# Kernel tuning notes

Measured on AMD Instinct MI355X. Metric: run time of the kernel, lower is better.

## Reference

```python
import jax, jax.numpy as jnp
import numpy as np

N, K, D = 100000, 8, 128
EPS = 1e-08


def setup_inputs() -> dict:
    key = jax.random.key(0)
    ks = jax.random.split(key, K)
    return {f"h{i}": jax.random.normal(ks[i], (N, D), dtype=jnp.float32) for i in range(K)}


def reference(h0, h1, h2, h3, h4, h5, h6, h7):
    # stack heads: [N, K, D] (matches torch.stack(head_outputs, dim=1))
    x = jnp.stack([h0, h1, h2, h3, h4, h5, h6, h7], axis=1)
    # F.normalize(p=2, dim=1, eps): x / max(||x||_2, eps) per (node, head) row
    norm = jnp.linalg.norm(x, axis=-1, keepdims=True)
    xn = x / jnp.maximum(norm, EPS)
    # per-node cross-correlation: [N, K, K]
    cc = jnp.einsum('nkd,nld->nkl', xn, xn)
    diff = cc - jnp.eye(K, dtype=cc.dtype)  # broadcasts over N
    # mean over nodes of sum of squared off-identity entries
    return jnp.sum(diff * diff) / N
```

## Files before the change

### kernel.cpp

```cpp
#include <hip/hip_runtime.h>


#define EPS 1e-8f

constexpr int D = 128;
constexpr int BLOCK = 64;
constexpr int NODES_PER_BLOCK = 16;

__global__ __launch_bounds__(BLOCK) void btd_main(
    const float* __restrict__ h0, const float* __restrict__ h1,
    const float* __restrict__ h2, const float* __restrict__ h3,
    const float* __restrict__ h4, const float* __restrict__ h5,
    const float* __restrict__ h6, const float* __restrict__ h7,
    float* __restrict__ partials, int n_nodes)
{
    const int lane = threadIdx.x & 63;
    const int g    = lane >> 2;
    const int l    = lane & 3;
    const int node = blockIdx.x * NODES_PER_BLOCK + g;

    float acc[36];
    #pragma unroll
    for (int i = 0; i < 36; ++i) acc[i] = 0.f;

    const unsigned base = (unsigned)node * D + l * 4;
    #pragma unroll
    for (int i = 0; i < 8; ++i) {
        const unsigned off = base + i * 16;
        float4 v[8];
        v[0] = *reinterpret_cast<const float4*>(h0 + off);
        v[1] = *reinterpret_cast<const float4*>(h1 + off);
        v[2] = *reinterpret_cast<const float4*>(h2 + off);
        v[3] = *reinterpret_cast<const float4*>(h3 + off);
        v[4] = *reinterpret_cast<const float4*>(h4 + off);
        v[5] = *reinterpret_cast<const float4*>(h5 + off);
        v[6] = *reinterpret_cast<const float4*>(h6 + off);
        v[7] = *reinterpret_cast<const float4*>(h7 + off);
        int idx = 0;
        #pragma unroll
        for (int k = 0; k < 8; ++k) {
            #pragma unroll
            for (int m = k; m < 8; ++m) {
                acc[idx] += v[k].x * v[m].x + v[k].y * v[m].y
                          + v[k].z * v[m].z + v[k].w * v[m].w;
                ++idx;
            }
        }
    }

    #pragma unroll
    for (int i = 0; i < 36; ++i) {
        acc[i] += __shfl_xor(acc[i], 1, 64);
        acc[i] += __shfl_xor(acc[i], 2, 64);
    }

    float inv[8];
    float loss = 0.f;
    #pragma unroll
    for (int k = 0; k < 8; ++k) {
        const int dk = k * (17 - k) / 2;
        inv[k] = rsqrtf(fmaxf(acc[dk], EPS * EPS));
        const float dterm = acc[dk] * inv[k] * inv[k] - 1.0f;
        loss += dterm * dterm;
    }
    #pragma unroll
    for (int k = 0; k < 8; ++k) {
        #pragma unroll
        for (int m = k + 1; m < 8; ++m) {
            const float cc = acc[k * (17 - k) / 2 + (m - k)] * inv[k] * inv[m];
            loss += 2.0f * cc * cc;
        }
    }
    loss *= 0.25f;

    #pragma unroll
    for (int off = 32; off > 0; off >>= 1)
        loss += __shfl_down(loss, off, 64);
    if (lane == 0) partials[blockIdx.x] = loss;
}

__global__ __launch_bounds__(256) void btd_reduce(
    const float* __restrict__ partials, int nparts,
    float* __restrict__ out, float inv_n)
{
    float s = 0.f;
    for (int i = threadIdx.x; i < nparts; i += 256) s += partials[i];
    #pragma unroll
    for (int off = 32; off > 0; off >>= 1) s += __shfl_down(s, off, 64);
    __shared__ float smem[4];
    const int lane = threadIdx.x & 63, wave = threadIdx.x >> 6;
    if (lane == 0) smem[wave] = s;
    __syncthreads();
    if (threadIdx.x == 0) out[0] = (smem[0] + smem[1] + smem[2] + smem[3]) * inv_n;
}

extern "C" void kernel_launch(void* const* d_in, const int* in_sizes, int n_in,
                              void* d_out, int out_size, void* d_ws, size_t ws_size,
                              hipStream_t stream) {
    const int n_nodes = in_sizes[0] / D;
    const int nblocks = (n_nodes + NODES_PER_BLOCK - 1) / NODES_PER_BLOCK;
    float* partials = (float*)d_ws;

    btd_main<<<nblocks, BLOCK, 0, stream>>>(
        (const float*)d_in[0], (const float*)d_in[1],
        (const float*)d_in[2], (const float*)d_in[3],
        (const float*)d_in[4], (const float*)d_in[5],
        (const float*)d_in[6], (const float*)d_in[7],
        partials, n_nodes);

    btd_reduce<<<1, 256, 0, stream>>>(partials, nblocks,
                                      (float*)d_out, 1.0f / (float)n_nodes);
}
```

Baseline: 88.73 us.

## Fuse final reduction via last-block atomic counter, double-buffer loads, enlarge blocks

Merges the separate reduce kernel into the main kernel. Each block writes its partial sum, bumps an atomic counter, and the last block to finish does the final sum. Blocks grow from one wave to four, with a shared-memory reduction across waves, and the per-node loads are double-buffered so the next chunk's loads are issued before the current chunk is accumulated. It adds a memset launch to reset the counter and keeps two register buffers live, which raises register pressure.

```diff
diff --git a/kernel.cpp b/kernel.cpp
--- a/kernel.cpp
+++ b/kernel.cpp
@@ -4,38 +4,48 @@
 #define EPS 1e-8f
 
 constexpr int D = 128;
-constexpr int BLOCK = 64;
-constexpr int NODES_PER_BLOCK = 16;
+constexpr int BLOCK = 256;
+constexpr int NODES_PER_BLOCK = 64;
 
-__global__ __launch_bounds__(BLOCK) void btd_main(
+__global__ __launch_bounds__(BLOCK) void btd_fused(
     const float* __restrict__ h0, const float* __restrict__ h1,
     const float* __restrict__ h2, const float* __restrict__ h3,
     const float* __restrict__ h4, const float* __restrict__ h5,
     const float* __restrict__ h6, const float* __restrict__ h7,
-    float* __restrict__ partials, int n_nodes)
+    float* __restrict__ ws, float* __restrict__ out,
+    int n_nodes, int nblocks)
 {
-    const int lane = threadIdx.x & 63;
+    unsigned* counter = (unsigned*)ws;
+    float* partials = ws + 16;
+
+    const int tid  = threadIdx.x;
+    const int lane = tid & 63;
+    const int wave = tid >> 6;
     const int g    = lane >> 2;
     const int l    = lane & 3;
-    const int node = blockIdx.x * NODES_PER_BLOCK + g;
+    int node = blockIdx.x * NODES_PER_BLOCK + wave * 16 + g;
+    const bool valid = (node < n_nodes);
+    if (!valid) node = n_nodes - 1;
 
     float acc[36];
     #pragma unroll
     for (int i = 0; i < 36; ++i) acc[i] = 0.f;
 
     const unsigned base = (unsigned)node * D + l * 4;
-    #pragma unroll
-    for (int i = 0; i < 8; ++i) {
+
+    float4 va[8], vb[8];
+    auto loadv = [&](float4* dst, int i) {
         const unsigned off = base + i * 16;
-        float4 v[8];
-        v[0] = *reinterpret_cast<const float4*>(h0 + off);
-        v[1] = *reinterpret_cast<const float4*>(h1 + off);
-        v[2] = *reinterpret_cast<const float4*>(h2 + off);
-        v[3] = *reinterpret_cast<const float4*>(h3 + off);
-        v[4] = *reinterpret_cast<const float4*>(h4 + off);
-        v[5] = *reinterpret_cast<const float4*>(h5 + off);
-        v[6] = *reinterpret_cast<const float4*>(h6 + off);
-        v[7] = *reinterpret_cast<const float4*>(h7 + off);
+        dst[0] = *reinterpret_cast<const float4*>(h0 + off);
+        dst[1] = *reinterpret_cast<const float4*>(h1 + off);
+        dst[2] = *reinterpret_cast<const float4*>(h2 + off);
+        dst[3] = *reinterpret_cast<const float4*>(h3 + off);
+        dst[4] = *reinterpret_cast<const float4*>(h4 + off);
+        dst[5] = *reinterpret_cast<const float4*>(h5 + off);
+        dst[6] = *reinterpret_cast<const float4*>(h6 + off);
+        dst[7] = *reinterpret_cast<const float4*>(h7 + off);
+    };
+    auto accv = [&](const float4* v) {
         int idx = 0;
         #pragma unroll
         for (int k = 0; k < 8; ++k) {
@@ -46,7 +56,18 @@
                 ++idx;
             }
         }
-    }
+    };
+
+    loadv(va, 0);
+    loadv(vb, 1);
+    accv(va);  loadv(va, 2);
+    accv(vb);  loadv(vb, 3);
+    accv(va);  loadv(va, 4);
+    accv(vb);  loadv(vb, 5);
+    accv(va);  loadv(va, 6);
+    accv(vb);  loadv(vb, 7);
+    accv(va);
+    accv(vb);
 
     #pragma unroll
     for (int i = 0; i < 36; ++i) {
@@ -71,27 +92,40 @@
             loss += 2.0f * cc * cc;
         }
     }
-    loss *= 0.25f;
+    loss = valid ? loss * 0.25f : 0.f;
 
     #pragma unroll
     for (int off = 32; off > 0; off >>= 1)
         loss += __shfl_down(loss, off, 64);
-    if (lane == 0) partials[blockIdx.x] = loss;
-}
 
-__global__ __launch_bounds__(256) void btd_reduce(
-    const float* __restrict__ partials, int nparts,
-    float* __restrict__ out, float inv_n)
-{
-    float s = 0.f;
-    for (int i = threadIdx.x; i < nparts; i += 256) s += partials[i];
-    #pragma unroll
-    for (int off = 32; off > 0; off >>= 1) s += __shfl_down(s, off, 64);
     __shared__ float smem[4];
-    const int lane = threadIdx.x & 63, wave = threadIdx.x >> 6;
-    if (lane == 0) smem[wave] = s;
+    __shared__ int lastFlag;
+    if (lane == 0) smem[wave] = loss;
     __syncthreads();
-    if (threadIdx.x == 0) out[0] = (smem[0] + smem[1] + smem[2] + smem[3]) * inv_n;
+    if (tid == 0) {
+        const float bsum = smem[0] + smem[1] + smem[2] + smem[3];
+        __hip_atomic_store(&partials[blockIdx.x], bsum,
+                           __ATOMIC_RELAXED, __HIP_MEMORY_SCOPE_AGENT);
+        __threadfence();
+        const unsigned old = atomicAdd(counter, 1u);
+        lastFlag = (old == (unsigned)(nblocks - 1));
+    }
+    __syncthreads();
+
+    if (lastFlag) {
+        __threadfence();
+        float s = 0.f;
+        for (int i = tid; i < nblocks; i += BLOCK)
+            s += __hip_atomic_load(&partials[i], __ATOMIC_RELAXED,
+                                   __HIP_MEMORY_SCOPE_AGENT);
+        #pragma unroll
+        for (int off = 32; off > 0; off >>= 1)
+            s += __shfl_down(s, off, 64);
+        if (lane == 0) smem[wave] = s;
+        __syncthreads();
+        if (tid == 0)
+            out[0] = (smem[0] + smem[1] + smem[2] + smem[3]) / (float)n_nodes;
+    }
 }
 
 extern "C" void kernel_launch(void* const* d_in, const int* in_sizes, int n_in,
@@ -99,15 +133,13 @@
                               hipStream_t stream) {
     const int n_nodes = in_sizes[0] / D;
     const int nblocks = (n_nodes + NODES_PER_BLOCK - 1) / NODES_PER_BLOCK;
-    float* partials = (float*)d_ws;
 
-    btd_main<<<nblocks, BLOCK, 0, stream>>>(
+    hipMemsetAsync(d_ws, 0, 64, stream);
+
+    btd_fused<<<nblocks, BLOCK, 0, stream>>>(
         (const float*)d_in[0], (const float*)d_in[1],
         (const float*)d_in[2], (const float*)d_in[3],
         (const float*)d_in[4], (const float*)d_in[5],
         (const float*)d_in[6], (const float*)d_in[7],
-        partials, n_nodes);
-
-    btd_reduce<<<1, 256, 0, stream>>>(partials, nblocks,
-                                      (float*)d_out, 1.0f / (float)n_nodes);
+        (float*)d_ws, (float*)d_out, n_nodes, nblocks);
 }
```

After: 176.0 us. 98.4% more time.
